# Kernel tuning notes

Hardware: AMD Instinct MI355X
Metric: run time of the kernel (lower is better)

The kernel has to match this reference:

```python
import jax, jax.numpy as jnp
import numpy as np
import math

NO_BLOCKS = 8; C_S = 384; C_Z = 128; C = 16; H = 12; PQ = 4; PV = 8
SCALE = 10.0; EPS = 1e-8; INF = 1e5; B = 1; N = 512
CAT = H*C + H*PV*3 + H*PV + H*C_Z  # 2112


def setup_inputs() -> dict:
    key = jax.random.key(0)
    ks = iter(jax.random.split(key, 64))
    def rn(shape, s=0.02):
        return (jax.random.normal(next(ks), shape, dtype=jnp.float32) * s)
    f32 = jnp.float32
    return dict(
        s=rn((B, N, C_S), 1.0), z=rn((B, N, N, C_Z), 1.0),
        rigid_quats=rn((B, N, 4), 1.0), rigid_trans=rn((B, N, 3), 1.0),
        mask=jnp.ones((B, N), f32),
        ln_s_g=jnp.ones((C_S,), f32), ln_s_b=jnp.zeros((C_S,), f32),
        ln_z_g=jnp.ones((C_Z,), f32), ln_z_b=jnp.zeros((C_Z,), f32),
        w_in=rn((C_S, C_S)), b_in=jnp.zeros((C_S,), f32),
        w_q=rn((H*C, C_S)), b_q=jnp.zeros((H*C,), f32),
        w_kv=rn((2*H*C, C_S)), b_kv=jnp.zeros((2*H*C,), f32),
        w_qp=rn((H*PQ*3, C_S)), b_qp=jnp.zeros((H*PQ*3,), f32),
        w_kvp=rn((H*(PQ+PV)*3, C_S)), b_kvp=jnp.zeros((H*(PQ+PV)*3,), f32),
        w_b=rn((H, C_Z)), b_b=jnp.zeros((H,), f32),
        head_weights=jnp.zeros((H,), f32),
        w_o=rn((C_S, CAT)), b_o=jnp.zeros((C_S,), f32),
        ln_ipa_g=jnp.ones((C_S,), f32), ln_ipa_b=jnp.zeros((C_S,), f32),
        ln_tr_g=jnp.ones((C_S,), f32), ln_tr_b=jnp.zeros((C_S,), f32),
        w_t1=rn((C_S, C_S)), b_t1=jnp.zeros((C_S,), f32),
        w_t2=rn((C_S, C_S)), b_t2=jnp.zeros((C_S,), f32),
        w_t3=rn((C_S, C_S)), b_t3=jnp.zeros((C_S,), f32),
        w_bb=rn((6, C_S)), b_bb=jnp.zeros((6,), f32),
    )


def _ln(x, g, b):
    m = jnp.mean(x, -1, keepdims=True)
    v = jnp.var(x, -1, keepdims=True)
    return (x - m) * jax.lax.rsqrt(v + 1e-5) * g + b


def _quat_to_rot(q):
    q = q / jnp.linalg.norm(q, axis=-1, keepdims=True)
    w, x, y, z = jnp.moveaxis(q, -1, 0)
    r00 = 1 - 2*(y*y + z*z); r01 = 2*(x*y - w*z); r02 = 2*(x*z + w*y)
    r10 = 2*(x*y + w*z); r11 = 1 - 2*(x*x + z*z); r12 = 2*(y*z - w*x)
    r20 = 2*(x*z - w*y); r21 = 2*(y*z + w*x); r22 = 1 - 2*(x*x + y*y)
    rows = jnp.stack([jnp.stack([r00, r01, r02], -1),
                      jnp.stack([r10, r11, r12], -1),
                      jnp.stack([r20, r21, r22], -1)], -2)
    return rows  # [..., 3, 3]


def _quat_mul(q, r):
    qw, qx, qy, qz = jnp.moveaxis(q, -1, 0)
    rw, rx, ry, rz = jnp.moveaxis(r, -1, 0)
    return jnp.stack([
        qw*rw - qx*rx - qy*ry - qz*rz,
        qw*rx + qx*rw + qy*rz - qz*ry,
        qw*ry - qx*rz + qy*rw + qz*rx,
        qw*rz + qx*ry - qy*rx + qz*rw], -1)


def _ipa(s, z, quats, trans, mask, p):
    rot = _quat_to_rot(quats)  # [B,N,3,3]
    q = (s @ p['w_q'].T + p['b_q']).reshape(B, N, H, C)
    kv = (s @ p['w_kv'].T + p['b_kv']).reshape(B, N, H, 2*C)
    k, v = kv[..., :C], kv[..., C:]
    def to_pts(lin_out, npts):
        pts = jnp.moveaxis(lin_out.reshape(B, N, 3, npts), -2, -1)  # split-into-3 layout -> [B,N,npts,3]
        pts = jnp.einsum('bnxy,bnpy->bnpx', rot, pts) + trans[:, :, None, :]
        return pts.reshape(B, N, H, npts // H, 3)
    q_pts = to_pts(s @ p['w_qp'].T + p['b_qp'], H*PQ)
    kv_pts = to_pts(s @ p['w_kvp'].T + p['b_kvp'], H*(PQ+PV))
    k_pts, v_pts = kv_pts[..., :PQ, :], kv_pts[..., PQ:, :]
    bpair = z @ p['w_b'].T + p['b_b']  # [B,N,N,H]
    a = jnp.einsum('bihc,bjhc->bhij', q, k) * math.sqrt(1.0 / (3 * C))
    a = a + math.sqrt(1.0 / 3.0) * jnp.moveaxis(bpair, -1, 1)
    d2 = jnp.sum((q_pts[:, :, None] - k_pts[:, None]) ** 2, -1)  # [B,N,N,H,PQ]
    hw = jax.nn.softplus(p['head_weights']) * math.sqrt(1.0 / (3 * (PQ * 9.0 / 2)))
    pt_att = -0.5 * jnp.sum(d2 * hw[None, None, None, :, None], -1)  # [B,N,N,H]
    a = a + jnp.moveaxis(pt_att, -1, 1)
    sq_mask = INF * (mask[:, :, None] * mask[:, None, :] - 1.0)
    a = jax.nn.softmax(a + sq_mask[:, None], -1)  # [B,H,N,N]
    o = jnp.einsum('bhij,bjhc->bihc', a, v).reshape(B, N, H * C)
    o_pt = jnp.einsum('bhij,bjhpx->bihpx', a, v_pts)  # [B,N,H,PV,3]
    o_pt_loc = jnp.einsum('bnyx,bnhpy->bnhpx', rot, o_pt - trans[:, :, None, None, :])
    o_pt_norm = jnp.sqrt(jnp.sum(o_pt_loc**2, -1) + EPS).reshape(B, N, H * PV)
    o_pair = jnp.einsum('bhij,bijc->bihc', a, z).reshape(B, N, H * C_Z)
    fl = o_pt_loc.reshape(B, N, H * PV, 3)
    cat = jnp.concatenate([o, fl[..., 0], fl[..., 1], fl[..., 2], o_pt_norm, o_pair], -1)
    return cat @ p['w_o'].T + p['b_o']


def reference(s, z, rigid_quats, rigid_trans, mask, ln_s_g, ln_s_b, ln_z_g, ln_z_b,
              w_in, b_in, w_q, b_q, w_kv, b_kv, w_qp, b_qp, w_kvp, b_kvp, w_b, b_b,
              head_weights, w_o, b_o, ln_ipa_g, ln_ipa_b, ln_tr_g, ln_tr_b,
              w_t1, b_t1, w_t2, b_t2, w_t3, b_t3, w_bb, b_bb):
    p = dict(w_q=w_q, b_q=b_q, w_kv=w_kv, b_kv=b_kv, w_qp=w_qp, b_qp=b_qp,
             w_kvp=w_kvp, b_kvp=b_kvp, w_b=w_b, b_b=b_b, head_weights=head_weights,
             w_o=w_o, b_o=b_o)
    s = _ln(s, ln_s_g, ln_s_b)
    z = _ln(z, ln_z_g, ln_z_b)
    s = s @ w_in.T + b_in
    quats = rigid_quats / jnp.linalg.norm(rigid_quats, axis=-1, keepdims=True)
    trans = rigid_trans / SCALE  # scale_translation(1/trans_scale_factor)
    frames = []
    for i in range(NO_BLOCKS):
        s = s + _ipa(s, z, quats, trans, mask, p)
        s = _ln(s, ln_ipa_g, ln_ipa_b)  # dropout is identity in eval
        t = jax.nn.relu(s @ w_t1.T + b_t1)
        t = jax.nn.relu(t @ w_t2.T + b_t2)
        s = s + (t @ w_t3.T + b_t3)
        s = _ln(s, ln_tr_g, ln_tr_b)
        upd = s @ w_bb.T + b_bb  # [B,N,6] backbone update
        rot = _quat_to_rot(quats)
        r_upd = jnp.concatenate([jnp.ones(upd.shape[:-1] + (1,), upd.dtype), upd[..., :3]], -1)
        quats = _quat_mul(quats, r_upd)
        quats = quats / jnp.linalg.norm(quats, axis=-1, keepdims=True)
        trans = trans + jnp.einsum('bnxy,bny->bnx', rot, upd[..., 3:])
        frames.append(jnp.concatenate([quats, trans * SCALE], -1))
        if i < NO_BLOCKS - 1:
            quats = jax.lax.stop_gradient(quats)  # stop_rot_gradient
    return jnp.stack(frames), s
```

## Files before the change

### kernel.cpp

```cpp
#include <hip/hip_runtime.h>
#include <math.h>

#define N_RES 512
#define CS 384
#define CZ 128
#define HD 12
#define CH 16
#define QKV_DIM 1152
#define CAT_DIM 2112
#define INF_F 100000.0f

typedef __attribute__((ext_vector_type(8))) __bf16 bf16x8;
typedef __attribute__((ext_vector_type(4))) float f32x4;

__device__ inline bf16x8 cvt8(float4 a, float4 b) {
    bf16x8 r;
    r[0] = (__bf16)a.x; r[1] = (__bf16)a.y; r[2] = (__bf16)a.z; r[3] = (__bf16)a.w;
    r[4] = (__bf16)b.x; r[5] = (__bf16)b.y; r[6] = (__bf16)b.z; r[7] = (__bf16)b.w;
    return r;
}

__device__ inline void quat_rot(float w, float x, float y, float z, float* r) {
    float n = 1.0f / sqrtf(w*w + x*x + y*y + z*z);
    w *= n; x *= n; y *= n; z *= n;
    r[0] = 1 - 2*(y*y + z*z); r[1] = 2*(x*y - w*z);     r[2] = 2*(x*z + w*y);
    r[3] = 2*(x*y + w*z);     r[4] = 1 - 2*(x*x + z*z); r[5] = 2*(y*z - w*x);
    r[6] = 2*(x*z - w*y);     r[7] = 2*(y*z + w*x);     r[8] = 1 - 2*(x*x + y*y);
}

__global__ __launch_bounds__(256) void gemm_mfma(
    const float* __restrict__ A, const float* __restrict__ W,
    const float* __restrict__ bias, const float* res, float* out,
    int M, int Nn, int K, int relu)
{
    __shared__ __bf16 Asl[64 * 64];
    __shared__ __bf16 Bsl[64 * 64];
    int bm = blockIdx.y * 64;
    int bn = blockIdx.x * 64;
    int tid = threadIdx.x;

    int tr = tid >> 2;
    int tu = (tid & 3) * 2;
    const float* ga0 = A + (size_t)(bm + tr) * K + tu * 8;
    const float* gb0 = W + (size_t)(bn + tr) * K + tu * 8;

    int lane = tid & 63;
    int w = tid >> 6;
    int wr = w >> 1, wc = w & 1;
    int lr = lane & 15, lg = lane >> 4;
    int arow0 = wr * 32 + lr, arow1 = arow0 + 16;
    int brow0 = wc * 32 + lr, brow1 = brow0 + 16;

    f32x4 acc00 = {0.f, 0.f, 0.f, 0.f}, acc01 = {0.f, 0.f, 0.f, 0.f};
    f32x4 acc10 = {0.f, 0.f, 0.f, 0.f}, acc11 = {0.f, 0.f, 0.f, 0.f};

    float4 ra0, ra1, ra2, ra3, rb0, rb1, rb2, rb3;
    ra0 = ((const float4*)ga0)[0]; ra1 = ((const float4*)ga0)[1];
    ra2 = ((const float4*)ga0)[2]; ra3 = ((const float4*)ga0)[3];
    rb0 = ((const float4*)gb0)[0]; rb1 = ((const float4*)gb0)[1];
    rb2 = ((const float4*)gb0)[2]; rb3 = ((const float4*)gb0)[3];

    int u0 = tu ^ (tr & 7);
    int u1 = (tu + 1) ^ (tr & 7);

    for (int k0 = 0; k0 < K; k0 += 64) {
        __syncthreads();
        *(bf16x8*)(Asl + tr * 64 + u0 * 8) = cvt8(ra0, ra1);
        *(bf16x8*)(Asl + tr * 64 + u1 * 8) = cvt8(ra2, ra3);
        *(bf16x8*)(Bsl + tr * 64 + u0 * 8) = cvt8(rb0, rb1);
        *(bf16x8*)(Bsl + tr * 64 + u1 * 8) = cvt8(rb2, rb3);
        __syncthreads();
        if (k0 + 64 < K) {
            const float* ga = ga0 + k0 + 64;
            const float* gb = gb0 + k0 + 64;
            ra0 = ((const float4*)ga)[0]; ra1 = ((const float4*)ga)[1];
            ra2 = ((const float4*)ga)[2]; ra3 = ((const float4*)ga)[3];
            rb0 = ((const float4*)gb)[0]; rb1 = ((const float4*)gb)[1];
            rb2 = ((const float4*)gb)[2]; rb3 = ((const float4*)gb)[3];
        }
        #pragma unroll
        for (int ks = 0; ks < 2; ++ks) {
            int ub = ks * 4 + lg;
            bf16x8 a0 = *(bf16x8*)(Asl + arow0 * 64 + (ub ^ (lr & 7)) * 8);
            bf16x8 a1 = *(bf16x8*)(Asl + arow1 * 64 + (ub ^ (lr & 7)) * 8);
            bf16x8 b0 = *(bf16x8*)(Bsl + brow0 * 64 + (ub ^ (lr & 7)) * 8);
            bf16x8 b1 = *(bf16x8*)(Bsl + brow1 * 64 + (ub ^ (lr & 7)) * 8);
            acc00 = __builtin_amdgcn_mfma_f32_16x16x32_bf16(a0, b0, acc00, 0, 0, 0);
            acc01 = __builtin_amdgcn_mfma_f32_16x16x32_bf16(a0, b1, acc01, 0, 0, 0);
            acc10 = __builtin_amdgcn_mfma_f32_16x16x32_bf16(a1, b0, acc10, 0, 0, 0);
            acc11 = __builtin_amdgcn_mfma_f32_16x16x32_bf16(a1, b1, acc11, 0, 0, 0);
        }
    }

    int mb = bm + wr * 32, nb = bn + wc * 32;
    #pragma unroll
    for (int fm = 0; fm < 2; ++fm) {
        #pragma unroll
        for (int fn = 0; fn < 2; ++fn) {
            f32x4 acc = fm == 0 ? (fn == 0 ? acc00 : acc01) : (fn == 0 ? acc10 : acc11);
            int n = nb + fn * 16 + lr;
            float bi = bias[n];
            int m0 = mb + fm * 16 + lg * 4;
            #pragma unroll
            for (int r = 0; r < 4; ++r) {
                float v = acc[r] + bi;
                if (res) v += res[(size_t)(m0 + r) * Nn + n];
                if (relu) v = fmaxf(v, 0.f);
                out[(size_t)(m0 + r) * Nn + n] = v;
            }
        }
    }
}

__global__ __launch_bounds__(64) void rowln_kernel(
    const float* in, float* out, const float* __restrict__ g, const float* __restrict__ b)
{
    int row = blockIdx.x;
    int lane = threadIdx.x;
    const float* x = in + (size_t)row * CS;
    float v[6];
    float s = 0.f, sq = 0.f;
    #pragma unroll
    for (int k = 0; k < 6; ++k) {
        v[k] = x[lane + k * 64];
        s += v[k]; sq += v[k] * v[k];
    }
    #pragma unroll
    for (int off = 32; off; off >>= 1) { s += __shfl_xor(s, off); sq += __shfl_xor(sq, off); }
    float mean = s * (1.0f / CS);
    float var = sq * (1.0f / CS) - mean * mean;
    float rstd = 1.0f / sqrtf(var + 1e-5f);
    float* o = out + (size_t)row * CS;
    #pragma unroll
    for (int k = 0; k < 6; ++k) {
        int c = lane + k * 64;
        o[c] = (v[k] - mean) * rstd * g[c] + b[c];
    }
}

__global__ __launch_bounds__(256) void zstats_kernel(const float* __restrict__ z, float* __restrict__ zstats)
{
    int wid = threadIdx.x >> 6;
    int lane = threadIdx.x & 63;
    size_t row = (size_t)blockIdx.x * 4 + wid;
    const float* x = z + row * CZ;
    float a = x[lane], b = x[lane + 64];
    float s = a + b, sq = a * a + b * b;
    #pragma unroll
    for (int off = 32; off; off >>= 1) { s += __shfl_xor(s, off); sq += __shfl_xor(sq, off); }
    if (lane == 0) {
        float mean = s * (1.0f / CZ);
        float var = sq * (1.0f / CZ) - mean * mean;
        zstats[row * 2] = mean;
        zstats[row * 2 + 1] = 1.0f / sqrtf(var + 1e-5f);
    }
}

__global__ __launch_bounds__(256) void bpair_kernel(
    const float* __restrict__ z, const float* __restrict__ zstats,
    const float* __restrict__ lng, const float* __restrict__ lnb,
    const float* __restrict__ w_b, const float* __restrict__ b_b,
    const float* __restrict__ mask, float* __restrict__ bpair)
{
    __shared__ float wbs[HD][CZ];
    __shared__ float gs[CZ], bs[CZ];
    for (int idx = threadIdx.x; idx < HD * CZ; idx += 256) wbs[idx / CZ][idx % CZ] = w_b[idx];
    if (threadIdx.x < CZ) { gs[threadIdx.x] = lng[threadIdx.x]; bs[threadIdx.x] = lnb[threadIdx.x]; }
    __syncthreads();
    size_t row = (size_t)blockIdx.x * 256 + threadIdx.x;
    int i = (int)(row >> 9), j = (int)(row & 511);
    const float* zr = z + row * CZ;
    float m = zstats[row * 2], r = zstats[row * 2 + 1];
    float acc[HD];
    #pragma unroll
    for (int h = 0; h < HD; ++h) acc[h] = 0.f;
    for (int c = 0; c < CZ; c += 4) {
        float4 zv = *(const float4*)(zr + c);
        float zn0 = (zv.x - m) * r * gs[c] + bs[c];
        float zn1 = (zv.y - m) * r * gs[c+1] + bs[c+1];
        float zn2 = (zv.z - m) * r * gs[c+2] + bs[c+2];
        float zn3 = (zv.w - m) * r * gs[c+3] + bs[c+3];
        #pragma unroll
        for (int h = 0; h < HD; ++h)
            acc[h] += zn0 * wbs[h][c] + zn1 * wbs[h][c+1] + zn2 * wbs[h][c+2] + zn3 * wbs[h][c+3];
    }
    float mterm = INF_F * (mask[i] * mask[j] - 1.0f);
    #pragma unroll
    for (int h = 0; h < HD; ++h)
        bpair[((size_t)h * N_RES + i) * N_RES + j] = 0.57735026919f * (acc[h] + b_b[h]) + mterm;
}

__global__ __launch_bounds__(256) void pack_kernel(
    const float* __restrict__ w_q, const float* __restrict__ w_kv,
    const float* __restrict__ w_qp, const float* __restrict__ w_kvp,
    const float* __restrict__ b_q, const float* __restrict__ b_kv,
    const float* __restrict__ b_qp, const float* __restrict__ b_kvp,
    float* __restrict__ wqkv, float* __restrict__ bqkv)
{
    int idx = blockIdx.x * 256 + threadIdx.x;
    if (idx < QKV_DIM * CS) {
        int rowi = idx / CS, col = idx % CS;
        float v;
        if (rowi < 192) v = w_q[rowi * CS + col];
        else if (rowi < 576) v = w_kv[(rowi - 192) * CS + col];
        else if (rowi < 720) v = w_qp[(rowi - 576) * CS + col];
        else v = w_kvp[(rowi - 720) * CS + col];
        wqkv[idx] = v;
    }
    if (idx < QKV_DIM) {
        float v;
        if (idx < 192) v = b_q[idx];
        else if (idx < 576) v = b_kv[idx - 192];
        else if (idx < 720) v = b_qp[idx - 576];
        else v = b_kvp[idx - 720];
        bqkv[idx] = v;
    }
}

__global__ void init_kernel(const float* __restrict__ rq, const float* __restrict__ rt,
                            float* __restrict__ quats, float* __restrict__ trans)
{
    int i = blockIdx.x * 256 + threadIdx.x;
    if (i < N_RES) {
        float w = rq[i*4], x = rq[i*4+1], y = rq[i*4+2], z = rq[i*4+3];
        float n = 1.0f / sqrtf(w*w + x*x + y*y + z*z);
        quats[i*4] = w*n; quats[i*4+1] = x*n; quats[i*4+2] = y*n; quats[i*4+3] = z*n;
        trans[i*3] = rt[i*3] * 0.1f; trans[i*3+1] = rt[i*3+1] * 0.1f; trans[i*3+2] = rt[i*3+2] * 0.1f;
    }
}

__global__ __launch_bounds__(192) void transform_kernel(
    const float* __restrict__ qkv, const float* __restrict__ quats, const float* __restrict__ trans,
    float* __restrict__ qpts, float* __restrict__ kpts, float* __restrict__ vcat)
{
    int i = blockIdx.x, t = threadIdx.x;
    float R[9];
    quat_rot(quats[i*4], quats[i*4+1], quats[i*4+2], quats[i*4+3], R);
    float tx = trans[i*3], ty = trans[i*3+1], tz = trans[i*3+2];
    const float* row = qkv + (size_t)i * QKV_DIM;
    if (t < 48) {
        float lx = row[576 + t], ly = row[576 + 48 + t], lz = row[576 + 96 + t];
        float gx = R[0]*lx + R[1]*ly + R[2]*lz + tx;
        float gy = R[3]*lx + R[4]*ly + R[5]*lz + ty;
        float gz = R[6]*lx + R[7]*ly + R[8]*lz + tz;
        float* o = qpts + (size_t)i * 144 + t * 3;
        o[0] = gx; o[1] = gy; o[2] = gz;
    }
    if (t < 144) {
        int h = t / 12, pp = t % 12;
        float lx = row[720 + t], ly = row[720 + 144 + t], lz = row[720 + 288 + t];
        float gx = R[0]*lx + R[1]*ly + R[2]*lz + tx;
        float gy = R[3]*lx + R[4]*ly + R[5]*lz + ty;
        float gz = R[6]*lx + R[7]*ly + R[8]*lz + tz;
        if (pp < 4) {
            float* o = kpts + (size_t)i * 144 + h * 12 + pp * 3;
            o[0] = gx; o[1] = gy; o[2] = gz;
        } else {
            float* o = vcat + (size_t)i * 480 + h * 40 + 16 + (pp - 4) * 3;
            o[0] = gx; o[1] = gy; o[2] = gz;
        }
    }
    {
        int h = t >> 4, c = t & 15;
        vcat[(size_t)i * 480 + h * 40 + c] = row[192 + h * 32 + 16 + c];
    }
}

__global__ __launch_bounds__(256) void attn_kernel(
    const float* __restrict__ qkv, const float* __restrict__ qpts, const float* __restrict__ kpts,
    const float* __restrict__ bpair, const float* __restrict__ head_weights, float* __restrict__ a)
{
    int i = blockIdx.x, h = blockIdx.y;
    __shared__ float qs[CH], qps[12], shw[1];
    __shared__ float redm[4], reds[4];
    int t = threadIdx.x;
    if (t < CH) qs[t] = qkv[(size_t)i * QKV_DIM + h * CH + t];
    else if (t < CH + 12) qps[t - CH] = qpts[(size_t)i * 144 + h * 12 + (t - CH)];
    else if (t == 31) {
        float x = head_weights[h];
        float sp = (x > 20.f) ? x : log1pf(expf(x));
        shw[0] = sp * 0.13608276348f;
    }
    __syncthreads();
    float hw = shw[0];
    float xv[2];
    #pragma unroll
    for (int r = 0; r < 2; ++r) {
        int j = t + r * 256;
        const float* kr = qkv + (size_t)j * QKV_DIM + 192 + h * 32;
        float dot = 0.f;
        #pragma unroll
        for (int c = 0; c < CH; ++c) dot += qs[c] * kr[c];
        const float* kp = kpts + (size_t)j * 144 + h * 12;
        float pt = 0.f;
        #pragma unroll
        for (int pc = 0; pc < 12; ++pc) { float d = qps[pc] - kp[pc]; pt += d * d; }
        xv[r] = dot * 0.14433756730f + bpair[((size_t)h * N_RES + i) * N_RES + j] - 0.5f * hw * pt;
    }
    float lm = fmaxf(xv[0], xv[1]);
    #pragma unroll
    for (int off = 32; off; off >>= 1) lm = fmaxf(lm, __shfl_xor(lm, off));
    if ((t & 63) == 0) redm[t >> 6] = lm;
    __syncthreads();
    float bmx = fmaxf(fmaxf(redm[0], redm[1]), fmaxf(redm[2], redm[3]));
    float e0 = expf(xv[0] - bmx), e1 = expf(xv[1] - bmx);
    float ls = e0 + e1;
    #pragma unroll
    for (int off = 32; off; off >>= 1) ls += __shfl_xor(ls, off);
    if ((t & 63) == 0) reds[t >> 6] = ls;
    __syncthreads();
    float inv = 1.0f / (reds[0] + reds[1] + reds[2] + reds[3]);
    float* arow = a + ((size_t)h * N_RES + i) * N_RES;
    arow[t] = e0 * inv;
    arow[t + 256] = e1 * inv;
}

__global__ __launch_bounds__(256) void ogemm_kernel(
    const float* __restrict__ a, const float* __restrict__ vcat, float* __restrict__ o_tmp)
{
    int h = blockIdx.y;
    int bm = blockIdx.x * 64;
    __shared__ float As[64][33];
    __shared__ float Vs[32][40];
    int t = threadIdx.x;
    int il_c = t & 63, ng = t >> 6;
    float acc[10];
    #pragma unroll
    for (int r = 0; r < 10; ++r) acc[r] = 0.f;
    for (int j0 = 0; j0 < N_RES; j0 += 32) {
        {
            int l = t * 8;
            int il = l >> 5, jl = l & 31;
            const float4* src = (const float4*)(a + ((size_t)h * N_RES + bm + il) * N_RES + j0 + jl);
            float4 v0 = src[0], v1 = src[1];
            As[il][jl]   = v0.x; As[il][jl+1] = v0.y; As[il][jl+2] = v0.z; As[il][jl+3] = v0.w;
            As[il][jl+4] = v1.x; As[il][jl+5] = v1.y; As[il][jl+6] = v1.z; As[il][jl+7] = v1.w;
        }
        #pragma unroll
        for (int r = 0; r < 5; ++r) {
            int l = t + 256 * r;
            int jj = l / 40, n = l % 40;
            Vs[jj][n] = vcat[(size_t)(j0 + jj) * 480 + h * 40 + n];
        }
        __syncthreads();
        #pragma unroll 8
        for (int jj = 0; jj < 32; ++jj) {
            float av = As[il_c][jj];
            #pragma unroll
            for (int r = 0; r < 10; ++r) acc[r] += av * Vs[jj][ng * 10 + r];
        }
        __syncthreads();
    }
    float* o = o_tmp + ((size_t)h * N_RES + bm + il_c) * 40 + ng * 10;
    #pragma unroll
    for (int r = 0; r < 10; ++r) o[r] = acc[r];
}

__global__ __launch_bounds__(512) void opair_kernel(
    const float* __restrict__ z, const float* __restrict__ zstats, const float* __restrict__ a,
    const float* __restrict__ lng, const float* __restrict__ lnb, float* __restrict__ cat)
{
    int i = blockIdx.x;
    int t = threadIdx.x;
    int c = t & 127, jg = t >> 7;
    __shared__ float als[HD][N_RES];
    __shared__ float zst[N_RES * 2];
    __shared__ float pacc[4][HD][CZ];
    for (int idx = t; idx < HD * N_RES; idx += 512) {
        int h = idx >> 9, j = idx & 511;
        als[h][j] = a[((size_t)h * N_RES + i) * N_RES + j];
    }
    for (int idx = t; idx < N_RES * 2; idx += 512) zst[idx] = zstats[(size_t)i * N_RES * 2 + idx];
    __syncthreads();
    float g = lng[c], b = lnb[c];
    float acc[HD];
    #pragma unroll
    for (int h = 0; h < HD; ++h) acc[h] = 0.f;
    const float* zr = z + ((size_t)i * N_RES + jg * 128) * CZ + c;
    for (int jj = 0; jj < 128; ++jj) {
        int j = jg * 128 + jj;
        float m = zst[j * 2], r = zst[j * 2 + 1];
        float zn = (zr[(size_t)jj * CZ] - m) * r * g + b;
        #pragma unroll
        for (int h = 0; h < HD; ++h) acc[h] += als[h][j] * zn;
    }
    #pragma unroll
    for (int h = 0; h < HD; ++h) pacc[jg][h][c] = acc[h];
    __syncthreads();
    #pragma unroll
    for (int k = 0; k < 3; ++k) {
        int idx = t + k * 512;
        int h = idx >> 7, cc = idx & 127;
        float v = pacc[0][h][cc] + pacc[1][h][cc] + pacc[2][h][cc] + pacc[3][h][cc];
        cat[(size_t)i * CAT_DIM + 576 + h * CZ + cc] = v;
    }
}

__global__ __launch_bounds__(192) void cat_kernel(
    const float* __restrict__ o_tmp, const float* __restrict__ quats, const float* __restrict__ trans,
    float* __restrict__ cat)
{
    int i = blockIdx.x, t = threadIdx.x;
    float R[9];
    quat_rot(quats[i*4], quats[i*4+1], quats[i*4+2], quats[i*4+3], R);
    float tx = trans[i*3], ty = trans[i*3+1], tz = trans[i*3+2];
    float* crow = cat + (size_t)i * CAT_DIM;
    {
        int h = t >> 4, c = t & 15;
        crow[t] = o_tmp[((size_t)h * N_RES + i) * 40 + c];
    }
    if (t < 96) {
        int h = t >> 3, p = t & 7;
        const float* og = o_tmp + ((size_t)h * N_RES + i) * 40 + 16 + p * 3;
        float dx = og[0] - tx, dy = og[1] - ty, dz = og[2] - tz;
        float lx = R[0]*dx + R[3]*dy + R[6]*dz;
        float ly = R[1]*dx + R[4]*dy + R[7]*dz;
        float lz = R[2]*dx + R[5]*dy + R[8]*dz;
        crow[192 + t] = lx;
        crow[288 + t] = ly;
        crow[384 + t] = lz;
        crow[480 + t] = sqrtf(lx*lx + ly*ly + lz*lz + 1e-8f);
    }
}

__global__ __launch_bounds__(256) void frame_kernel(
    const float* __restrict__ s, const float* __restrict__ w_bb, const float* __restrict__ b_bb,
    float* quats, float* trans, float* __restrict__ frames_out)
{
    int lane = threadIdx.x & 63;
    int i = (blockIdx.x * 256 + threadIdx.x) >> 6;
    const float* srow = s + (size_t)i * CS;
    float p[6];
    #pragma unroll
    for (int r = 0; r < 6; ++r) p[r] = 0.f;
    #pragma unroll
    for (int k = 0; k < 6; ++k) {
        int c = lane + k * 64;
        float sv = srow[c];
        #pragma unroll
        for (int r = 0; r < 6; ++r) p[r] += sv * w_bb[r * CS + c];
    }
    #pragma unroll
    for (int r = 0; r < 6; ++r)
        #pragma unroll
        for (int off = 32; off; off >>= 1) p[r] += __shfl_xor(p[r], off);
    if (lane == 0) {
        float u0 = p[0] + b_bb[0], u1 = p[1] + b_bb[1], u2 = p[2] + b_bb[2];
        float u3 = p[3] + b_bb[3], u4 = p[4] + b_bb[4], u5 = p[5] + b_bb[5];
        float qw = quats[i*4], qx = quats[i*4+1], qy = quats[i*4+2], qz = quats[i*4+3];
        float R[9];
        quat_rot(qw, qx, qy, qz, R);
        float nw = qw - qx*u0 - qy*u1 - qz*u2;
        float nx = qw*u0 + qx + qy*u2 - qz*u1;
        float ny = qw*u1 - qx*u2 + qy + qz*u0;
        float nz = qw*u2 + qx*u1 - qy*u0 + qz;
        float n = 1.0f / sqrtf(nw*nw + nx*nx + ny*ny + nz*nz);
        nw *= n; nx *= n; ny *= n; nz *= n;
        float t0 = trans[i*3+0] + R[0]*u3 + R[1]*u4 + R[2]*u5;
        float t1 = trans[i*3+1] + R[3]*u3 + R[4]*u4 + R[5]*u5;
        float t2 = trans[i*3+2] + R[6]*u3 + R[7]*u4 + R[8]*u5;
        quats[i*4] = nw; quats[i*4+1] = nx; quats[i*4+2] = ny; quats[i*4+3] = nz;
        trans[i*3] = t0; trans[i*3+1] = t1; trans[i*3+2] = t2;
        float* f = frames_out + (size_t)i * 7;
        f[0] = nw; f[1] = nx; f[2] = ny; f[3] = nz;
        f[4] = t0 * 10.f; f[5] = t1 * 10.f; f[6] = t2 * 10.f;
    }
}

extern "C" void kernel_launch(void* const* d_in, const int* in_sizes, int n_in,
                              void* d_out, int out_size, void* d_ws, size_t ws_size,
                              hipStream_t stream)
{
    const float* s_in  = (const float*)d_in[0];
    const float* z     = (const float*)d_in[1];
    const float* rq    = (const float*)d_in[2];
    const float* rt    = (const float*)d_in[3];
    const float* mask  = (const float*)d_in[4];
    const float* ln_s_g = (const float*)d_in[5];
    const float* ln_s_b = (const float*)d_in[6];
    const float* ln_z_g = (const float*)d_in[7];
    const float* ln_z_b = (const float*)d_in[8];
    const float* w_in  = (const float*)d_in[9];
    const float* b_in  = (const float*)d_in[10];
    const float* w_q   = (const float*)d_in[11];
    const float* b_q   = (const float*)d_in[12];
    const float* w_kv  = (const float*)d_in[13];
    const float* b_kv  = (const float*)d_in[14];
    const float* w_qp  = (const float*)d_in[15];
    const float* b_qp  = (const float*)d_in[16];
    const float* w_kvp = (const float*)d_in[17];
    const float* b_kvp = (const float*)d_in[18];
    const float* w_b   = (const float*)d_in[19];
    const float* b_b   = (const float*)d_in[20];
    const float* head_weights = (const float*)d_in[21];
    const float* w_o   = (const float*)d_in[22];
    const float* b_o   = (const float*)d_in[23];
    const float* ln_ipa_g = (const float*)d_in[24];
    const float* ln_ipa_b = (const float*)d_in[25];
    const float* ln_tr_g  = (const float*)d_in[26];
    const float* ln_tr_b  = (const float*)d_in[27];
    const float* w_t1  = (const float*)d_in[28];
    const float* b_t1  = (const float*)d_in[29];
    const float* w_t2  = (const float*)d_in[30];
    const float* b_t2  = (const float*)d_in[31];
    const float* w_t3  = (const float*)d_in[32];
    const float* b_t3  = (const float*)d_in[33];
    const float* w_bb  = (const float*)d_in[34];
    const float* b_bb  = (const float*)d_in[35];

    float* ws = (float*)d_ws;
    size_t off = 0;
    auto alloc = [&](size_t n) { float* p = ws + off; off += n; return p; };
    float* s_tmp   = alloc((size_t)N_RES * CS);
    float* t1      = alloc((size_t)N_RES * CS);
    float* t2      = alloc((size_t)N_RES * CS);
    float* zstats  = alloc((size_t)N_RES * N_RES * 2);
    float* bpair   = alloc((size_t)HD * N_RES * N_RES);
    float* abuf    = alloc((size_t)HD * N_RES * N_RES);
    float* qkv_all = alloc((size_t)N_RES * QKV_DIM);
    float* qpts    = alloc((size_t)N_RES * 144);
    float* kpts    = alloc((size_t)N_RES * 144);
    float* vcat    = alloc((size_t)N_RES * 480);
    float* o_tmp   = alloc((size_t)HD * N_RES * 40);
    float* cat     = alloc((size_t)N_RES * CAT_DIM);
    float* quats   = alloc((size_t)N_RES * 4);
    float* trans   = alloc((size_t)N_RES * 3 + 1);
    float* wqkv    = alloc((size_t)QKV_DIM * CS);
    float* bqkv    = alloc((size_t)QKV_DIM);
    float* s_cur   = alloc((size_t)N_RES * CS);
    (void)ws_size; (void)in_sizes; (void)n_in; (void)out_size;

    init_kernel<<<2, 256, 0, stream>>>(rq, rt, quats, trans);
    rowln_kernel<<<N_RES, 64, 0, stream>>>(s_in, s_tmp, ln_s_g, ln_s_b);
    gemm_mfma<<<dim3(CS / 64, N_RES / 64), 256, 0, stream>>>(s_tmp, w_in, b_in, nullptr, s_cur, N_RES, CS, CS, 0);
    zstats_kernel<<<(N_RES * N_RES) / 4, 256, 0, stream>>>(z, zstats);
    bpair_kernel<<<(N_RES * N_RES) / 256, 256, 0, stream>>>(z, zstats, ln_z_g, ln_z_b, w_b, b_b, mask, bpair);
    pack_kernel<<<(QKV_DIM * CS + 255) / 256, 256, 0, stream>>>(w_q, w_kv, w_qp, w_kvp, b_q, b_kv, b_qp, b_kvp, wqkv, bqkv);

    float* frames = (float*)d_out;
    for (int it = 0; it < 8; ++it) {
        gemm_mfma<<<dim3(QKV_DIM / 64, N_RES / 64), 256, 0, stream>>>(s_cur, wqkv, bqkv, nullptr, qkv_all, N_RES, QKV_DIM, CS, 0);
        transform_kernel<<<N_RES, 192, 0, stream>>>(qkv_all, quats, trans, qpts, kpts, vcat);
        attn_kernel<<<dim3(N_RES, HD), 256, 0, stream>>>(qkv_all, qpts, kpts, bpair, head_weights, abuf);
        ogemm_kernel<<<dim3(N_RES / 64, HD), 256, 0, stream>>>(abuf, vcat, o_tmp);
        opair_kernel<<<N_RES, 512, 0, stream>>>(z, zstats, abuf, ln_z_g, ln_z_b, cat);
        cat_kernel<<<N_RES, 192, 0, stream>>>(o_tmp, quats, trans, cat);
        gemm_mfma<<<dim3(CS / 64, N_RES / 64), 256, 0, stream>>>(cat, w_o, b_o, s_cur, s_cur, N_RES, CS, CAT_DIM, 0);
        rowln_kernel<<<N_RES, 64, 0, stream>>>(s_cur, s_cur, ln_ipa_g, ln_ipa_b);
        gemm_mfma<<<dim3(CS / 64, N_RES / 64), 256, 0, stream>>>(s_cur, w_t1, b_t1, nullptr, t1, N_RES, CS, CS, 1);
        gemm_mfma<<<dim3(CS / 64, N_RES / 64), 256, 0, stream>>>(t1, w_t2, b_t2, nullptr, t2, N_RES, CS, CS, 1);
        gemm_mfma<<<dim3(CS / 64, N_RES / 64), 256, 0, stream>>>(t2, w_t3, b_t3, s_cur, s_cur, N_RES, CS, CS, 0);
        rowln_kernel<<<N_RES, 64, 0, stream>>>(s_cur, s_cur, ln_tr_g, ln_tr_b);
        frame_kernel<<<N_RES / 4, 256, 0, stream>>>(s_cur, w_bb, b_bb, quats, trans, frames + (size_t)it * N_RES * 7);
    }
    hipMemcpyAsync(frames + 8 * N_RES * 7, s_cur, sizeof(float) * N_RES * CS,
                   hipMemcpyDeviceToDevice, stream);
}
```

Measured before the change: 2.114 ms.

## Fuse attention softmax, value gemm, pair output and concat into one kernel

Merges attn_kernel, ogemm_kernel, opair_kernel and cat_kernel into a single per-residue kernel with 512 threads. All 12 heads' softmax rows stay in LDS instead of a 12x512x512 attention buffer in global memory, and the outputs go straight into cat. This removes the write and reread of the attention matrix and three kernel launches per block. In exchange, each block covers only one residue across all heads, giving 512 blocks, and the key reads are strided per thread rather than coalesced per head.

```diff
diff --git a/kernel.cpp b/kernel.cpp
--- a/kernel.cpp
+++ b/kernel.cpp
@@ -266,160 +266,136 @@
     }
 }
 
-__global__ __launch_bounds__(256) void attn_kernel(
+#define ALS_LD (N_RES + 1)
+__global__ __launch_bounds__(512) void fused_attn_kernel(
     const float* __restrict__ qkv, const float* __restrict__ qpts, const float* __restrict__ kpts,
-    const float* __restrict__ bpair, const float* __restrict__ head_weights, float* __restrict__ a)
-{
-    int i = blockIdx.x, h = blockIdx.y;
-    __shared__ float qs[CH], qps[12], shw[1];
-    __shared__ float redm[4], reds[4];
-    int t = threadIdx.x;
-    if (t < CH) qs[t] = qkv[(size_t)i * QKV_DIM + h * CH + t];
-    else if (t < CH + 12) qps[t - CH] = qpts[(size_t)i * 144 + h * 12 + (t - CH)];
-    else if (t == 31) {
-        float x = head_weights[h];
-        float sp = (x > 20.f) ? x : log1pf(expf(x));
-        shw[0] = sp * 0.13608276348f;
-    }
-    __syncthreads();
-    float hw = shw[0];
-    float xv[2];
-    #pragma unroll
-    for (int r = 0; r < 2; ++r) {
-        int j = t + r * 256;
-        const float* kr = qkv + (size_t)j * QKV_DIM + 192 + h * 32;
-        float dot = 0.f;
-        #pragma unroll
-        for (int c = 0; c < CH; ++c) dot += qs[c] * kr[c];
-        const float* kp = kpts + (size_t)j * 144 + h * 12;
-        float pt = 0.f;
-        #pragma unroll
-        for (int pc = 0; pc < 12; ++pc) { float d = qps[pc] - kp[pc]; pt += d * d; }
-        xv[r] = dot * 0.14433756730f + bpair[((size_t)h * N_RES + i) * N_RES + j] - 0.5f * hw * pt;
-    }
-    float lm = fmaxf(xv[0], xv[1]);
-    #pragma unroll
-    for (int off = 32; off; off >>= 1) lm = fmaxf(lm, __shfl_xor(lm, off));
-    if ((t & 63) == 0) redm[t >> 6] = lm;
-    __syncthreads();
-    float bmx = fmaxf(fmaxf(redm[0], redm[1]), fmaxf(redm[2], redm[3]));
-    float e0 = expf(xv[0] - bmx), e1 = expf(xv[1] - bmx);
-    float ls = e0 + e1;
-    #pragma unroll
-    for (int off = 32; off; off >>= 1) ls += __shfl_xor(ls, off);
-    if ((t & 63) == 0) reds[t >> 6] = ls;
-    __syncthreads();
-    float inv = 1.0f / (reds[0] + reds[1] + reds[2] + reds[3]);
-    float* arow = a + ((size_t)h * N_RES + i) * N_RES;
-    arow[t] = e0 * inv;
-    arow[t + 256] = e1 * inv;
-}
-
-__global__ __launch_bounds__(256) void ogemm_kernel(
-    const float* __restrict__ a, const float* __restrict__ vcat, float* __restrict__ o_tmp)
-{
-    int h = blockIdx.y;
-    int bm = blockIdx.x * 64;
-    __shared__ float As[64][33];
-    __shared__ float Vs[32][40];
-    int t = threadIdx.x;
-    int il_c = t & 63, ng = t >> 6;
-    float acc[10];
-    #pragma unroll
-    for (int r = 0; r < 10; ++r) acc[r] = 0.f;
-    for (int j0 = 0; j0 < N_RES; j0 += 32) {
-        {
-            int l = t * 8;
-            int il = l >> 5, jl = l & 31;
-            const float4* src = (const float4*)(a + ((size_t)h * N_RES + bm + il) * N_RES + j0 + jl);
-            float4 v0 = src[0], v1 = src[1];
-            As[il][jl]   = v0.x; As[il][jl+1] = v0.y; As[il][jl+2] = v0.z; As[il][jl+3] = v0.w;
-            As[il][jl+4] = v1.x; As[il][jl+5] = v1.y; As[il][jl+6] = v1.z; As[il][jl+7] = v1.w;
-        }
-        #pragma unroll
-        for (int r = 0; r < 5; ++r) {
-            int l = t + 256 * r;
-            int jj = l / 40, n = l % 40;
-            Vs[jj][n] = vcat[(size_t)(j0 + jj) * 480 + h * 40 + n];
-        }
-        __syncthreads();
-        #pragma unroll 8
-        for (int jj = 0; jj < 32; ++jj) {
-            float av = As[il_c][jj];
-            #pragma unroll
-            for (int r = 0; r < 10; ++r) acc[r] += av * Vs[jj][ng * 10 + r];
-        }
-        __syncthreads();
-    }
-    float* o = o_tmp + ((size_t)h * N_RES + bm + il_c) * 40 + ng * 10;
-    #pragma unroll
-    for (int r = 0; r < 10; ++r) o[r] = acc[r];
-}
-
-__global__ __launch_bounds__(512) void opair_kernel(
-    const float* __restrict__ z, const float* __restrict__ zstats, const float* __restrict__ a,
-    const float* __restrict__ lng, const float* __restrict__ lnb, float* __restrict__ cat)
+    const float* __restrict__ bpair, const float* __restrict__ head_weights,
+    const float* __restrict__ z, const float* __restrict__ zstats,
+    const float* __restrict__ lng, const float* __restrict__ lnb,
+    const float* __restrict__ vcat, const float* __restrict__ quats, const float* __restrict__ trans,
+    float* __restrict__ cat)
 {
     int i = blockIdx.x;
     int t = threadIdx.x;
-    int c = t & 127, jg = t >> 7;
-    __shared__ float als[HD][N_RES];
+    __shared__ float als[HD][ALS_LD];
+    __shared__ float qs[HD * CH];
+    __shared__ float qp[144];
+    __shared__ float shw[HD];
+    __shared__ float red[HD][8];
+    __shared__ float o_lds[480];
     __shared__ float zst[N_RES * 2];
-    __shared__ float pacc[4][HD][CZ];
-    for (int idx = t; idx < HD * N_RES; idx += 512) {
-        int h = idx >> 9, j = idx & 511;
-        als[h][j] = a[((size_t)h * N_RES + i) * N_RES + j];
+
+    if (t < 192) qs[t] = qkv[(size_t)i * QKV_DIM + t];
+    else if (t < 336) qp[t - 192] = qpts[(size_t)i * 144 + (t - 192)];
+    else if (t < 348) {
+        float x = head_weights[t - 336];
+        float sp = (x > 20.f) ? x : log1pf(expf(x));
+        shw[t - 336] = sp * 0.13608276348f;
     }
     for (int idx = t; idx < N_RES * 2; idx += 512) zst[idx] = zstats[(size_t)i * N_RES * 2 + idx];
     __syncthreads();
-    float g = lng[c], b = lnb[c];
-    float acc[HD];
-    #pragma unroll
-    for (int h = 0; h < HD; ++h) acc[h] = 0.f;
-    const float* zr = z + ((size_t)i * N_RES + jg * 128) * CZ + c;
-    for (int jj = 0; jj < 128; ++jj) {
-        int j = jg * 128 + jj;
-        float m = zst[j * 2], r = zst[j * 2 + 1];
-        float zn = (zr[(size_t)jj * CZ] - m) * r * g + b;
-        #pragma unroll
-        for (int h = 0; h < HD; ++h) acc[h] += als[h][j] * zn;
-    }
-    #pragma unroll
-    for (int h = 0; h < HD; ++h) pacc[jg][h][c] = acc[h];
-    __syncthreads();
-    #pragma unroll
-    for (int k = 0; k < 3; ++k) {
-        int idx = t + k * 512;
-        int h = idx >> 7, cc = idx & 127;
-        float v = pacc[0][h][cc] + pacc[1][h][cc] + pacc[2][h][cc] + pacc[3][h][cc];
-        cat[(size_t)i * CAT_DIM + 576 + h * CZ + cc] = v;
-    }
-}
-
-__global__ __launch_bounds__(192) void cat_kernel(
-    const float* __restrict__ o_tmp, const float* __restrict__ quats, const float* __restrict__ trans,
-    float* __restrict__ cat)
-{
-    int i = blockIdx.x, t = threadIdx.x;
-    float R[9];
-    quat_rot(quats[i*4], quats[i*4+1], quats[i*4+2], quats[i*4+3], R);
-    float tx = trans[i*3], ty = trans[i*3+1], tz = trans[i*3+2];
+
+    float x[HD];
+    {
+        const float* kr = qkv + (size_t)t * QKV_DIM + 192;
+        const float* kp = kpts + (size_t)t * 144;
+        #pragma unroll
+        for (int h = 0; h < HD; ++h) {
+            float dot = 0.f;
+            #pragma unroll
+            for (int c = 0; c < CH; ++c) dot += qs[h * CH + c] * kr[h * 32 + c];
+            float pt = 0.f;
+            #pragma unroll
+            for (int pc = 0; pc < 12; ++pc) { float d = qp[h * 12 + pc] - kp[h * 12 + pc]; pt += d * d; }
+            x[h] = dot * 0.14433756730f + bpair[((size_t)h * N_RES + i) * N_RES + t] - 0.5f * shw[h] * pt;
+        }
+    }
+    int lane = t & 63, wv = t >> 6;
+    #pragma unroll
+    for (int h = 0; h < HD; ++h) {
+        float m = x[h];
+        #pragma unroll
+        for (int off = 32; off; off >>= 1) m = fmaxf(m, __shfl_xor(m, off));
+        if (lane == 0) red[h][wv] = m;
+    }
+    __syncthreads();
+    float ex[HD];
+    #pragma unroll
+    for (int h = 0; h < HD; ++h) {
+        float m = red[h][0];
+        #pragma unroll
+        for (int w2 = 1; w2 < 8; ++w2) m = fmaxf(m, red[h][w2]);
+        ex[h] = expf(x[h] - m);
+    }
+    __syncthreads();
+    #pragma unroll
+    for (int h = 0; h < HD; ++h) {
+        float s = ex[h];
+        #pragma unroll
+        for (int off = 32; off; off >>= 1) s += __shfl_xor(s, off);
+        if (lane == 0) red[h][wv] = s;
+    }
+    __syncthreads();
+    #pragma unroll
+    for (int h = 0; h < HD; ++h) {
+        float s = red[h][0] + red[h][1] + red[h][2] + red[h][3]
+                + red[h][4] + red[h][5] + red[h][6] + red[h][7];
+        als[h][t] = ex[h] * (1.0f / s);
+    }
+    __syncthreads();
+
+    if (t < 480) {
+        int h = t / 40, n = t % 40;
+        float a0 = 0.f, a1 = 0.f, a2 = 0.f, a3 = 0.f;
+        const float* vb = vcat + h * 40 + n;
+        for (int j = 0; j < N_RES; j += 4) {
+            a0 += als[h][j]     * vb[(size_t)(j)     * 480];
+            a1 += als[h][j + 1] * vb[(size_t)(j + 1) * 480];
+            a2 += als[h][j + 2] * vb[(size_t)(j + 2) * 480];
+            a3 += als[h][j + 3] * vb[(size_t)(j + 3) * 480];
+        }
+        o_lds[t] = (a0 + a1) + (a2 + a3);
+    }
+
+    {
+        int c = t & 127;
+        int h0 = t >> 7;
+        float g = lng[c], b = lnb[c];
+        float acc0 = 0.f, acc1 = 0.f, acc2 = 0.f;
+        const float* zr = z + (size_t)i * N_RES * CZ + c;
+        for (int j = 0; j < N_RES; ++j) {
+            float m = zst[j * 2], r = zst[j * 2 + 1];
+            float zn = (zr[(size_t)j * CZ] - m) * r * g + b;
+            acc0 += als[h0][j] * zn;
+            acc1 += als[h0 + 4][j] * zn;
+            acc2 += als[h0 + 8][j] * zn;
+        }
+        float* o = cat + (size_t)i * CAT_DIM + 576;
+        o[h0 * CZ + c] = acc0;
+        o[(h0 + 4) * CZ + c] = acc1;
+        o[(h0 + 8) * CZ + c] = acc2;
+    }
+    __syncthreads();
+
     float* crow = cat + (size_t)i * CAT_DIM;
-    {
+    if (t < 192) {
         int h = t >> 4, c = t & 15;
-        crow[t] = o_tmp[((size_t)h * N_RES + i) * 40 + c];
-    }
-    if (t < 96) {
-        int h = t >> 3, p = t & 7;
-        const float* og = o_tmp + ((size_t)h * N_RES + i) * 40 + 16 + p * 3;
+        crow[t] = o_lds[h * 40 + c];
+    } else if (t < 288) {
+        int tt = t - 192;
+        int h = tt >> 3, p = tt & 7;
+        float R[9];
+        quat_rot(quats[i*4], quats[i*4+1], quats[i*4+2], quats[i*4+3], R);
+        float tx = trans[i*3], ty = trans[i*3+1], tz = trans[i*3+2];
+        const float* og = o_lds + h * 40 + 16 + p * 3;
         float dx = og[0] - tx, dy = og[1] - ty, dz = og[2] - tz;
         float lx = R[0]*dx + R[3]*dy + R[6]*dz;
         float ly = R[1]*dx + R[4]*dy + R[7]*dz;
         float lz = R[2]*dx + R[5]*dy + R[8]*dz;
-        crow[192 + t] = lx;
-        crow[288 + t] = ly;
-        crow[384 + t] = lz;
-        crow[480 + t] = sqrtf(lx*lx + ly*ly + lz*lz + 1e-8f);
+        crow[192 + tt] = lx;
+        crow[288 + tt] = ly;
+        crow[384 + tt] = lz;
+        crow[480 + tt] = sqrtf(lx*lx + ly*ly + lz*lz + 1e-8f);
     }
 }
 
@@ -516,12 +492,10 @@
     float* t2      = alloc((size_t)N_RES * CS);
     float* zstats  = alloc((size_t)N_RES * N_RES * 2);
     float* bpair   = alloc((size_t)HD * N_RES * N_RES);
-    float* abuf    = alloc((size_t)HD * N_RES * N_RES);
     float* qkv_all = alloc((size_t)N_RES * QKV_DIM);
     float* qpts    = alloc((size_t)N_RES * 144);
     float* kpts    = alloc((size_t)N_RES * 144);
     float* vcat    = alloc((size_t)N_RES * 480);
-    float* o_tmp   = alloc((size_t)HD * N_RES * 40);
     float* cat     = alloc((size_t)N_RES * CAT_DIM);
     float* quats   = alloc((size_t)N_RES * 4);
     float* trans   = alloc((size_t)N_RES * 3 + 1);
@@ -541,10 +515,8 @@
     for (int it = 0; it < 8; ++it) {
         gemm_mfma<<<dim3(QKV_DIM / 64, N_RES / 64), 256, 0, stream>>>(s_cur, wqkv, bqkv, nullptr, qkv_all, N_RES, QKV_DIM, CS, 0);
         transform_kernel<<<N_RES, 192, 0, stream>>>(qkv_all, quats, trans, qpts, kpts, vcat);
-        attn_kernel<<<dim3(N_RES, HD), 256, 0, stream>>>(qkv_all, qpts, kpts, bpair, head_weights, abuf);
-        ogemm_kernel<<<dim3(N_RES / 64, HD), 256, 0, stream>>>(abuf, vcat, o_tmp);
-        opair_kernel<<<N_RES, 512, 0, stream>>>(z, zstats, abuf, ln_z_g, ln_z_b, cat);
-        cat_kernel<<<N_RES, 192, 0, stream>>>(o_tmp, quats, trans, cat);
+        fused_attn_kernel<<<N_RES, 512, 0, stream>>>(qkv_all, qpts, kpts, bpair, head_weights,
+                                                     z, zstats, ln_z_g, ln_z_b, vcat, quats, trans, cat);
         gemm_mfma<<<dim3(CS / 64, N_RES / 64), 256, 0, stream>>>(cat, w_o, b_o, s_cur, s_cur, N_RES, CS, CAT_DIM, 0);
         rowln_kernel<<<N_RES, 64, 0, stream>>>(s_cur, s_cur, ln_ipa_g, ln_ipa_b);
         gemm_mfma<<<dim3(CS / 64, N_RES / 64), 256, 0, stream>>>(s_cur, w_t1, b_t1, nullptr, t1, N_RES, CS, CS, 1);
```

Result: slower. 4.239 ms (+100.5%).
